# Performance work log

Measured on AMD Instinct MI355X. Metric: run time of the kernel, lower is better.

## Reference

```python
import jax, jax.numpy as jnp
import numpy as np


def setup_inputs() -> dict:
    key = jax.random.key(0)
    k1, k2, k3 = jax.random.split(key, 3)
    B, C, E = 65536, 32, 512
    candidate_ids = jax.random.randint(k1, (B, C), 0, E, dtype=jnp.int64)
    candidate_scores = jax.random.uniform(k2, (B, C), dtype=jnp.float32)
    cooc = jax.random.uniform(k3, (E, E), dtype=jnp.float32)
    # row-normalize like update_cooccurrence would maintain
    cooc = cooc / jnp.clip(cooc.sum(axis=1, keepdims=True), 1e-8)
    return {
        "candidate_ids": candidate_ids,
        "candidate_scores": candidate_scores,
        "cooccurrence": cooc,
        "target_size": 64,
    }


def reference(candidate_ids, candidate_scores, cooccurrence, target_size):
    B, C = candidate_ids.shape
    E = cooccurrence.shape[0]
    num_to_add = target_size - C  # static; original returns early if <= 0
    rows = jnp.arange(B)[:, None]  # [B,1]
    # sum_i score[b,i] * cooccurrence[ids[b,i]]  ==  scatter scores into [B,E], then matmul
    sparse_scores = jnp.zeros((B, E), jnp.float32).at[rows, candidate_ids].add(candidate_scores)
    cooc_scores = sparse_scores @ cooccurrence  # [B,E]
    # mask out existing candidates
    cooc_scores = cooc_scores.at[rows, candidate_ids].set(-jnp.inf)
    additional_scores, additional_ids = jax.lax.top_k(cooc_scores, num_to_add)
    expanded_ids = jnp.concatenate([candidate_ids, additional_ids.astype(candidate_ids.dtype)], axis=-1)
    expanded_scores = jnp.concatenate([candidate_scores, additional_scores], axis=-1)
    return expanded_ids, expanded_scores
```

## Files before the change

kernel.cpp:

```cpp
#include <hip/hip_runtime.h>
#include <stdint.h>

typedef unsigned long long u64;
typedef unsigned int u32;

constexpr int Ccand = 32;
constexpr int Evoc  = 512;
constexpr int Tgt   = 64;

__device__ __forceinline__ void sort64_desc_f32(float& a, int lane) {
    #pragma unroll
    for (int k2 = 2; k2 <= 64; k2 <<= 1) {
        #pragma unroll
        for (int j = k2 >> 1; j > 0; j >>= 1) {
            float o = __shfl_xor(a, j);
            bool lower = (lane & j) == 0;
            bool keepMax = ((lane & k2) == 0) ? lower : !lower;
            bool g = a > o;
            a = (keepMax == g) ? a : o;
        }
    }
}

__device__ __forceinline__ void sort64_desc_u64(u64& a, int lane) {
    #pragma unroll
    for (int k2 = 2; k2 <= 64; k2 <<= 1) {
        #pragma unroll
        for (int j = k2 >> 1; j > 0; j >>= 1) {
            u64 o = __shfl_xor(a, j);
            bool lower = (lane & j) == 0;
            bool keepMax = ((lane & k2) == 0) ? lower : !lower;
            bool g = a > o;
            a = (keepMax == g) ? a : o;
        }
    }
}

__global__ __launch_bounds__(256, 4) void cooc_expand(
    const int* __restrict__ cand_ids,
    const float* __restrict__ cand_scores,
    const float* __restrict__ cooc,
    float* __restrict__ out_ids,
    float* __restrict__ out_scores,
    int B)
{
    const int lane = threadIdx.x & 63;
    const int wid  = threadIdx.x >> 6;
    const int row  = blockIdx.x * 4 + wid;
    __shared__ u64 buf[4][512];
    __shared__ u32 wmask[4][16];
    if (row >= B) return;

    if (lane < 16) wmask[wid][lane] = 0u;

    int   my_id = -1;
    float my_s  = 0.0f;
    if (lane < Ccand) {
        my_id = cand_ids[(size_t)row * Ccand + lane];
        my_s  = cand_scores[(size_t)row * Ccand + lane];
    }

    int   first = 64;
    float sm    = 0.0f;
    #pragma unroll
    for (int j = 0; j < Ccand; ++j) {
        int   idj = __shfl(my_id, j);
        float sj  = __shfl(my_s,  j);
        bool match = (idj == my_id);
        if (match && j < first) first = j;
        sm += match ? sj : 0.0f;
    }
    bool alive = (lane < Ccand) && (first == lane);
    u64 aball = __ballot(alive);
    int m = __popcll(aball);

    __threadfence_block();
    if (alive) atomicOr(&wmask[wid][my_id >> 5], 1u << (my_id & 31));
    __threadfence_block();

    u32 wword = wmask[wid][lane & 15];
    u32 pc = __popc(wword);
    u32 incl = pc;
    #pragma unroll
    for (int i = 1; i < 16; i <<= 1) {
        u32 t2 = __shfl_up(incl, i);
        if (lane >= i) incl += t2;
    }
    u32 scanex = incl - pc;
    int W = (my_id >> 5) & 15;
    u32 basew = __shfl(scanex, W);
    u32 wordw = __shfl(wword, W);
    int rk = (int)basew + __popc(wordw & ((1u << (my_id & 31)) - 1u));

    int dst = alive ? rk : ((lane < 32) ? (lane + 32) : lane);
    int sorted_id = __builtin_amdgcn_ds_permute(dst << 2, my_id);
    int sorted_sb = __builtin_amdgcn_ds_permute(dst << 2, __float_as_int(sm));

    float acc[8] = {0.f,0.f,0.f,0.f,0.f,0.f,0.f,0.f};
    const int l4 = lane << 2;
    #pragma unroll 1
    for (int t = 0; t < 32; t += 8) {
        int   e[8];
        float s[8];
        #pragma unroll
        for (int u = 0; u < 8; ++u) {
            e[u] = __builtin_amdgcn_readlane(sorted_id, t + u) & 511;
            s[u] = (t + u < m) ? __int_as_float(__builtin_amdgcn_readlane(sorted_sb, t + u)) : 0.0f;
        }
        float4 A[8], Bv[8];
        #pragma unroll
        for (int u = 0; u < 8; ++u) {
            const float* rp = cooc + ((size_t)e[u] << 9);
            A[u]  = *reinterpret_cast<const float4*>(rp + l4);
            Bv[u] = *reinterpret_cast<const float4*>(rp + 256 + l4);
        }
        #pragma unroll
        for (int u = 0; u < 8; ++u) {
            acc[0] = fmaf(s[u], A[u].x,  acc[0]);
            acc[1] = fmaf(s[u], A[u].y,  acc[1]);
            acc[2] = fmaf(s[u], A[u].z,  acc[2]);
            acc[3] = fmaf(s[u], A[u].w,  acc[3]);
            acc[4] = fmaf(s[u], Bv[u].x, acc[4]);
            acc[5] = fmaf(s[u], Bv[u].y, acc[5]);
            acc[6] = fmaf(s[u], Bv[u].z, acc[6]);
            acc[7] = fmaf(s[u], Bv[u].w, acc[7]);
        }
    }

    u32 wlo = __shfl(wword, lane >> 3);
    u32 whi = __shfl(wword, 8 + (lane >> 3));
    int sh = (lane & 7) << 2;
    u32 flo = (wlo >> sh) & 0xFu;
    u32 fhi = (whi >> sh) & 0xFu;

    float v[8];
    #pragma unroll
    for (int j = 0; j < 4; ++j) {
        v[j]     = ((flo >> j) & 1u) ? -1.0f : acc[j];
        v[4 + j] = ((fhi >> j) & 1u) ? -1.0f : acc[4 + j];
    }

    float mx8 = v[0];
    #pragma unroll
    for (int j = 1; j < 8; ++j) mx8 = fmaxf(mx8, v[j]);
    float srt = mx8;
    sort64_desc_f32(srt, lane);
    float L32 = __int_as_float(__builtin_amdgcn_readlane(__float_as_int(srt), 31));

    int cnt = 0;
    #pragma unroll
    for (int j = 0; j < 8; ++j) cnt += (v[j] >= L32) ? 1 : 0;
    u32 sincl = (u32)cnt;
    #pragma unroll
    for (int i = 1; i < 64; i <<= 1) {
        u32 t2 = __shfl_up(sincl, i);
        if (lane >= i) sincl += t2;
    }
    int sbase = (int)sincl - cnt;
    int S_tot = __builtin_amdgcn_readlane((int)sincl, 63);

    int slot = sbase;
    #pragma unroll
    for (int j = 0; j < 8; ++j) {
        bool s = (v[j] >= L32);
        if (s) {
            int col = (j < 4) ? (l4 + j) : (256 + l4 + (j - 4));
            buf[wid][slot] = ((u64)__float_as_uint(v[j]) << 32) | (u32)(511 - col);
        }
        slot += s ? 1 : 0;
    }
    __threadfence_block();

    u64 k;
    if (S_tot <= 64) {
        k = (lane < S_tot) ? buf[wid][lane] : 0ull;
        sort64_desc_u64(k, lane);
    } else {
        u64 cur = (lane < S_tot) ? buf[wid][lane] : 0ull;
        sort64_desc_u64(cur, lane);
        for (int base = 64; base < S_tot; base += 64) {
            u64 nxt = (base + lane < S_tot) ? buf[wid][base + lane] : 0ull;
            sort64_desc_u64(nxt, lane);
            u64 o = __shfl_xor(nxt, 63);
            cur = (cur >= o) ? cur : o;
            #pragma unroll
            for (int j = 32; j > 0; j >>= 1) {
                u64 p = __shfl_xor(cur, j);
                bool keepMax = (lane & j) == 0;
                bool g = cur > p;
                cur = (keepMax == g) ? cur : p;
            }
        }
        k = cur;
    }

    int src = (lane >= 32) ? (lane - 32) : 0;
    u64 kk = __shfl(k, src);
    const size_t ob = (size_t)row * Tgt;
    float oid, osc;
    if (lane < Ccand) {
        oid = (float)my_id;
        osc = my_s;
    } else {
        oid = (float)(int)(511 - (u32)(kk & 511ull));
        osc = __uint_as_float((u32)(kk >> 32));
    }
    out_ids[ob + lane]    = oid;
    out_scores[ob + lane] = osc;
}

extern "C" void kernel_launch(void* const* d_in, const int* in_sizes, int n_in,
                              void* d_out, int out_size, void* d_ws, size_t ws_size,
                              hipStream_t stream) {
    const int*   ids    = (const int*)d_in[0];
    const float* scores = (const float*)d_in[1];
    const float* cooc   = (const float*)d_in[2];
    int B = in_sizes[0] / Ccand;
    float* out_ids    = (float*)d_out;
    float* out_scores = out_ids + (size_t)B * Tgt;
    int blocks = (B + 3) / 4;
    hipLaunchKernelGGL(cooc_expand, dim3(blocks), dim3(256), 0, stream,
                       ids, scores, cooc, out_ids, out_scores, B);
}
```

Baseline: 215.1 us.

## Replace LDS bitmask dedup with sort-based dedup and packed FMA accumulation

Candidate deduplication now uses a 32-lane bitonic sort on (id,lane) keys with neighbor checks, falling back to an O(C) shuffle path only when an id appears three or more times. This removes the shared-memory bitmask, its atomics and the fences. The accumulation uses float2 vector FMAs so the compiler can emit packed FMA instructions. The existing-candidate mask is now built per lane inside the gather loop. The trade-off is more shuffle work in the sort and a data-dependent branch.

```diff
diff --git a/kernel.cpp b/kernel.cpp
--- a/kernel.cpp
+++ b/kernel.cpp
@@ -3,6 +3,7 @@
 
 typedef unsigned long long u64;
 typedef unsigned int u32;
+typedef float vf2 __attribute__((ext_vector_type(2)));
 
 constexpr int Ccand = 32;
 constexpr int Evoc  = 512;
@@ -48,10 +49,7 @@
     const int wid  = threadIdx.x >> 6;
     const int row  = blockIdx.x * 4 + wid;
     __shared__ u64 buf[4][512];
-    __shared__ u32 wmask[4][16];
     if (row >= B) return;
-
-    if (lane < 16) wmask[wid][lane] = 0u;
 
     int   my_id = -1;
     float my_s  = 0.0f;
@@ -60,43 +58,80 @@
         my_s  = cand_scores[(size_t)row * Ccand + lane];
     }
 
-    int   first = 64;
-    float sm    = 0.0f;
-    #pragma unroll
-    for (int j = 0; j < Ccand; ++j) {
-        int   idj = __shfl(my_id, j);
-        float sj  = __shfl(my_s,  j);
-        bool match = (idj == my_id);
-        if (match && j < first) first = j;
-        sm += match ? sj : 0.0f;
-    }
-    bool alive = (lane < Ccand) && (first == lane);
-    u64 aball = __ballot(alive);
-    int m = __popcll(aball);
-
-    __threadfence_block();
-    if (alive) atomicOr(&wmask[wid][my_id >> 5], 1u << (my_id & 31));
-    __threadfence_block();
-
-    u32 wword = wmask[wid][lane & 15];
-    u32 pc = __popc(wword);
-    u32 incl = pc;
-    #pragma unroll
-    for (int i = 1; i < 16; i <<= 1) {
-        u32 t2 = __shfl_up(incl, i);
-        if (lane >= i) incl += t2;
-    }
-    u32 scanex = incl - pc;
-    int W = (my_id >> 5) & 15;
-    u32 basew = __shfl(scanex, W);
-    u32 wordw = __shfl(wword, W);
-    int rk = (int)basew + __popc(wordw & ((1u << (my_id & 31)) - 1u));
-
-    int dst = alive ? rk : ((lane < 32) ? (lane + 32) : lane);
-    int sorted_id = __builtin_amdgcn_ds_permute(dst << 2, my_id);
-    int sorted_sb = __builtin_amdgcn_ds_permute(dst << 2, __float_as_int(sm));
-
-    float acc[8] = {0.f,0.f,0.f,0.f,0.f,0.f,0.f,0.f};
+    u32   key = (lane < Ccand) ? (((u32)my_id << 5) | (u32)lane) : 0x7FFFFFFFu;
+    float sv  = my_s;
+    const int l5 = lane & 31;
+    #pragma unroll
+    for (int k2 = 2; k2 <= 32; k2 <<= 1) {
+        #pragma unroll
+        for (int j = k2 >> 1; j > 0; j >>= 1) {
+            u32   ok = __shfl_xor(key, j);
+            float os = __shfl_xor(sv, j);
+            bool lower   = (l5 & j) == 0;
+            bool keepMin = ((l5 & k2) == 0) ? lower : !lower;
+            bool g = key < ok;
+            bool keep = (g == keepMin);
+            key = keep ? key : ok;
+            sv  = keep ? sv  : os;
+        }
+    }
+    int sid = (int)(key >> 5);
+    u32 kprev  = __shfl_up(key, 1);
+    u32 kprev2 = __shfl_up(key, 2);
+    u32 knext  = __shfl_down(key, 1);
+    float snext = __shfl_down(sv, 1);
+    int idprev  = (int)(kprev  >> 5);
+    int idprev2 = (int)(kprev2 >> 5);
+    int idnext  = (int)(knext  >> 5);
+    bool isFirst = (lane == 0) || (sid != idprev);
+    bool hasPair = (lane < 31) && (idnext == sid);
+    float ssum = sv + (hasPair ? snext : 0.0f);
+    bool third = (lane >= 2) && (lane < Ccand) && (sid == idprev) && (sid == idprev2);
+    bool anyTriple = (__ballot(third) != 0ull);
+
+    int sorted_id, sorted_sb, m;
+    if (!anyTriple) {
+        bool flag = (lane < Ccand) && isFirst;
+        int f = flag ? 1 : 0;
+        u32 inc = (u32)f;
+        #pragma unroll
+        for (int i = 1; i < 64; i <<= 1) {
+            u32 t2 = __shfl_up(inc, i);
+            if (lane >= i) inc += t2;
+        }
+        m = __builtin_amdgcn_readlane((int)inc, 63);
+        int dstl = flag ? ((int)inc - 1) : 63;
+        sorted_id = __builtin_amdgcn_ds_permute(dstl << 2, sid);
+        sorted_sb = __builtin_amdgcn_ds_permute(dstl << 2, __float_as_int(ssum));
+    } else {
+        int first = 64; float sm = 0.0f;
+        #pragma unroll
+        for (int j = 0; j < Ccand; ++j) {
+            int   idj = __shfl(my_id, j);
+            float sj  = __shfl(my_s,  j);
+            bool match = (idj == my_id);
+            if (match && j < first) first = j;
+            sm += match ? sj : 0.0f;
+        }
+        bool alive = (lane < Ccand) && (first == lane);
+        u64 ab = __ballot(alive);
+        m = __popcll(ab);
+        int rk = 0;
+        #pragma unroll
+        for (int j = 0; j < Ccand; ++j) {
+            int idj = __shfl(my_id, j);
+            bool aj = (ab >> j) & 1ull;
+            rk += (aj && idj < my_id) ? 1 : 0;
+        }
+        int dstl = alive ? rk : ((lane < 32) ? (lane + 32) : lane);
+        sorted_id = __builtin_amdgcn_ds_permute(dstl << 2, my_id);
+        sorted_sb = __builtin_amdgcn_ds_permute(dstl << 2, __float_as_int(sm));
+    }
+
+    vf2 acc2[4];
+    acc2[0] = (vf2){0.f, 0.f}; acc2[1] = (vf2){0.f, 0.f};
+    acc2[2] = (vf2){0.f, 0.f}; acc2[3] = (vf2){0.f, 0.f};
+    u32 maskbits = 0;
     const int l4 = lane << 2;
     #pragma unroll 1
     for (int t = 0; t < 32; t += 8) {
@@ -116,29 +151,29 @@
         }
         #pragma unroll
         for (int u = 0; u < 8; ++u) {
-            acc[0] = fmaf(s[u], A[u].x,  acc[0]);
-            acc[1] = fmaf(s[u], A[u].y,  acc[1]);
-            acc[2] = fmaf(s[u], A[u].z,  acc[2]);
-            acc[3] = fmaf(s[u], A[u].w,  acc[3]);
-            acc[4] = fmaf(s[u], Bv[u].x, acc[4]);
-            acc[5] = fmaf(s[u], Bv[u].y, acc[5]);
-            acc[6] = fmaf(s[u], Bv[u].z, acc[6]);
-            acc[7] = fmaf(s[u], Bv[u].w, acc[7]);
-        }
-    }
-
-    u32 wlo = __shfl(wword, lane >> 3);
-    u32 whi = __shfl(wword, 8 + (lane >> 3));
-    int sh = (lane & 7) << 2;
-    u32 flo = (wlo >> sh) & 0xFu;
-    u32 fhi = (whi >> sh) & 0xFu;
+            vf2 sv2; sv2[0] = s[u]; sv2[1] = s[u];
+            vf2 a0; a0[0] = A[u].x;  a0[1] = A[u].y;
+            vf2 a1; a1[0] = A[u].z;  a1[1] = A[u].w;
+            vf2 b0; b0[0] = Bv[u].x; b0[1] = Bv[u].y;
+            vf2 b1; b1[0] = Bv[u].z; b1[1] = Bv[u].w;
+            acc2[0] = __builtin_elementwise_fma(sv2, a0, acc2[0]);
+            acc2[1] = __builtin_elementwise_fma(sv2, a1, acc2[1]);
+            acc2[2] = __builtin_elementwise_fma(sv2, b0, acc2[2]);
+            acc2[3] = __builtin_elementwise_fma(sv2, b1, acc2[3]);
+        }
+        #pragma unroll
+        for (int u = 0; u < 8; ++u) {
+            if ((t + u < m) && (((e[u] & 255) >> 2) == lane))
+                maskbits |= 1u << (((e[u] >> 8) << 2) | (e[u] & 3));
+        }
+    }
 
     float v[8];
-    #pragma unroll
-    for (int j = 0; j < 4; ++j) {
-        v[j]     = ((flo >> j) & 1u) ? -1.0f : acc[j];
-        v[4 + j] = ((fhi >> j) & 1u) ? -1.0f : acc[4 + j];
-    }
+    v[0] = acc2[0][0]; v[1] = acc2[0][1]; v[2] = acc2[1][0]; v[3] = acc2[1][1];
+    v[4] = acc2[2][0]; v[5] = acc2[2][1]; v[6] = acc2[3][0]; v[7] = acc2[3][1];
+    #pragma unroll
+    for (int j = 0; j < 8; ++j)
+        if ((maskbits >> j) & 1u) v[j] = -1.0f;
 
     float mx8 = v[0];
     #pragma unroll
```

New measurement: 226.4 us. +5.3%, slower.

## Shrink LDS footprint, compute ranks and exclusion mask in registers, use packed FMA

Applied to the files above, without the earlier changes.

Replaces the shared-memory bitmask and atomicOr ranking with a register-only rank computed by shuffles over the alive candidates. The exclusion mask is now built per lane inside the gather loop. The top-k staging buffer is cut from 512 to 64 entries per wave by processing the threshold survivors in 64-element chunks, and launch bounds move from 4 to 8 blocks per CU. The inner loop now loads 4 rows per step instead of 8 and uses packed 2-wide FMAs. The intent is higher occupancy through less LDS and register pressure, at the cost of fewer loads in flight per wave, a 32-step shuffle loop, and re-scanning candidates for each chunk when more than 64 survive.

```diff
diff --git a/kernel.cpp b/kernel.cpp
--- a/kernel.cpp
+++ b/kernel.cpp
@@ -3,6 +3,7 @@
 
 typedef unsigned long long u64;
 typedef unsigned int u32;
+typedef float vf2 __attribute__((ext_vector_type(2)));
 
 constexpr int Ccand = 32;
 constexpr int Evoc  = 512;
@@ -36,7 +37,7 @@
     }
 }
 
-__global__ __launch_bounds__(256, 4) void cooc_expand(
+__global__ __launch_bounds__(256, 8) void cooc_expand(
     const int* __restrict__ cand_ids,
     const float* __restrict__ cand_scores,
     const float* __restrict__ cooc,
@@ -47,11 +48,8 @@
     const int lane = threadIdx.x & 63;
     const int wid  = threadIdx.x >> 6;
     const int row  = blockIdx.x * 4 + wid;
-    __shared__ u64 buf[4][512];
-    __shared__ u32 wmask[4][16];
+    __shared__ u64 buf[4][64];
     if (row >= B) return;
-
-    if (lane < 16) wmask[wid][lane] = 0u;
 
     int   my_id = -1;
     float my_s  = 0.0f;
@@ -74,71 +72,63 @@
     u64 aball = __ballot(alive);
     int m = __popcll(aball);
 
-    __threadfence_block();
-    if (alive) atomicOr(&wmask[wid][my_id >> 5], 1u << (my_id & 31));
-    __threadfence_block();
-
-    u32 wword = wmask[wid][lane & 15];
-    u32 pc = __popc(wword);
-    u32 incl = pc;
-    #pragma unroll
-    for (int i = 1; i < 16; i <<= 1) {
-        u32 t2 = __shfl_up(incl, i);
-        if (lane >= i) incl += t2;
-    }
-    u32 scanex = incl - pc;
-    int W = (my_id >> 5) & 15;
-    u32 basew = __shfl(scanex, W);
-    u32 wordw = __shfl(wword, W);
-    int rk = (int)basew + __popc(wordw & ((1u << (my_id & 31)) - 1u));
-
+    int rk = 0;
+    #pragma unroll
+    for (int j = 0; j < Ccand; ++j) {
+        int idj = __shfl(my_id, j);
+        bool aj = (aball >> j) & 1ull;
+        rk += (aj && idj < my_id) ? 1 : 0;
+    }
     int dst = alive ? rk : ((lane < 32) ? (lane + 32) : lane);
     int sorted_id = __builtin_amdgcn_ds_permute(dst << 2, my_id);
     int sorted_sb = __builtin_amdgcn_ds_permute(dst << 2, __float_as_int(sm));
 
-    float acc[8] = {0.f,0.f,0.f,0.f,0.f,0.f,0.f,0.f};
+    vf2 acc2[4];
+    acc2[0] = (vf2){0.f, 0.f}; acc2[1] = (vf2){0.f, 0.f};
+    acc2[2] = (vf2){0.f, 0.f}; acc2[3] = (vf2){0.f, 0.f};
+    u32 maskbits = 0;
     const int l4 = lane << 2;
     #pragma unroll 1
-    for (int t = 0; t < 32; t += 8) {
-        int   e[8];
-        float s[8];
-        #pragma unroll
-        for (int u = 0; u < 8; ++u) {
+    for (int t = 0; t < 32; t += 4) {
+        int   e[4];
+        float s[4];
+        #pragma unroll
+        for (int u = 0; u < 4; ++u) {
             e[u] = __builtin_amdgcn_readlane(sorted_id, t + u) & 511;
             s[u] = (t + u < m) ? __int_as_float(__builtin_amdgcn_readlane(sorted_sb, t + u)) : 0.0f;
         }
-        float4 A[8], Bv[8];
-        #pragma unroll
-        for (int u = 0; u < 8; ++u) {
+        float4 A[4], Bv[4];
+        #pragma unroll
+        for (int u = 0; u < 4; ++u) {
             const float* rp = cooc + ((size_t)e[u] << 9);
             A[u]  = *reinterpret_cast<const float4*>(rp + l4);
             Bv[u] = *reinterpret_cast<const float4*>(rp + 256 + l4);
         }
         #pragma unroll
-        for (int u = 0; u < 8; ++u) {
-            acc[0] = fmaf(s[u], A[u].x,  acc[0]);
-            acc[1] = fmaf(s[u], A[u].y,  acc[1]);
-            acc[2] = fmaf(s[u], A[u].z,  acc[2]);
-            acc[3] = fmaf(s[u], A[u].w,  acc[3]);
-            acc[4] = fmaf(s[u], Bv[u].x, acc[4]);
-            acc[5] = fmaf(s[u], Bv[u].y, acc[5]);
-            acc[6] = fmaf(s[u], Bv[u].z, acc[6]);
-            acc[7] = fmaf(s[u], Bv[u].w, acc[7]);
-        }
-    }
-
-    u32 wlo = __shfl(wword, lane >> 3);
-    u32 whi = __shfl(wword, 8 + (lane >> 3));
-    int sh = (lane & 7) << 2;
-    u32 flo = (wlo >> sh) & 0xFu;
-    u32 fhi = (whi >> sh) & 0xFu;
+        for (int u = 0; u < 4; ++u) {
+            vf2 sv2; sv2[0] = s[u]; sv2[1] = s[u];
+            vf2 a0; a0[0] = A[u].x;  a0[1] = A[u].y;
+            vf2 a1; a1[0] = A[u].z;  a1[1] = A[u].w;
+            vf2 b0; b0[0] = Bv[u].x; b0[1] = Bv[u].y;
+            vf2 b1; b1[0] = Bv[u].z; b1[1] = Bv[u].w;
+            acc2[0] = __builtin_elementwise_fma(sv2, a0, acc2[0]);
+            acc2[1] = __builtin_elementwise_fma(sv2, a1, acc2[1]);
+            acc2[2] = __builtin_elementwise_fma(sv2, b0, acc2[2]);
+            acc2[3] = __builtin_elementwise_fma(sv2, b1, acc2[3]);
+        }
+        #pragma unroll
+        for (int u = 0; u < 4; ++u) {
+            if ((t + u < m) && (((e[u] & 255) >> 2) == lane))
+                maskbits |= 1u << (((e[u] >> 8) << 2) | (e[u] & 3));
+        }
+    }
 
     float v[8];
-    #pragma unroll
-    for (int j = 0; j < 4; ++j) {
-        v[j]     = ((flo >> j) & 1u) ? -1.0f : acc[j];
-        v[4 + j] = ((fhi >> j) & 1u) ? -1.0f : acc[4 + j];
-    }
+    v[0] = acc2[0][0]; v[1] = acc2[0][1]; v[2] = acc2[1][0]; v[3] = acc2[1][1];
+    v[4] = acc2[2][0]; v[5] = acc2[2][1]; v[6] = acc2[3][0]; v[7] = acc2[3][1];
+    #pragma unroll
+    for (int j = 0; j < 8; ++j)
+        if ((maskbits >> j) & 1u) v[j] = -1.0f;
 
     float mx8 = v[0];
     #pragma unroll
@@ -159,28 +149,29 @@
     int sbase = (int)sincl - cnt;
     int S_tot = __builtin_amdgcn_readlane((int)sincl, 63);
 
-    int slot = sbase;
-    #pragma unroll
-    for (int j = 0; j < 8; ++j) {
-        bool s = (v[j] >= L32);
-        if (s) {
-            int col = (j < 4) ? (l4 + j) : (256 + l4 + (j - 4));
-            buf[wid][slot] = ((u64)__float_as_uint(v[j]) << 32) | (u32)(511 - col);
-        }
-        slot += s ? 1 : 0;
-    }
-    __threadfence_block();
-
-    u64 k;
-    if (S_tot <= 64) {
-        k = (lane < S_tot) ? buf[wid][lane] : 0ull;
-        sort64_desc_u64(k, lane);
-    } else {
-        u64 cur = (lane < S_tot) ? buf[wid][lane] : 0ull;
-        sort64_desc_u64(cur, lane);
-        for (int base = 64; base < S_tot; base += 64) {
-            u64 nxt = (base + lane < S_tot) ? buf[wid][base + lane] : 0ull;
-            sort64_desc_u64(nxt, lane);
+    int nchunk = (S_tot + 63) >> 6;
+    u64 cur = 0ull;
+    #pragma unroll 1
+    for (int c = 0; c < nchunk; ++c) {
+        const int lo = c << 6;
+        int slot = sbase;
+        #pragma unroll
+        for (int j = 0; j < 8; ++j) {
+            bool s = (v[j] >= L32);
+            int  rel = slot - lo;
+            if (s && rel >= 0 && rel < 64) {
+                int col = (j < 4) ? (l4 + j) : (256 + l4 + (j - 4));
+                buf[wid][rel] = ((u64)__float_as_uint(v[j]) << 32) | (u32)(511 - col);
+            }
+            slot += s ? 1 : 0;
+        }
+        __threadfence_block();
+        u64 nxt = (lo + lane < S_tot) ? buf[wid][lane] : 0ull;
+        __threadfence_block();
+        sort64_desc_u64(nxt, lane);
+        if (c == 0) {
+            cur = nxt;
+        } else {
             u64 o = __shfl_xor(nxt, 63);
             cur = (cur >= o) ? cur : o;
             #pragma unroll
@@ -191,11 +182,10 @@
                 cur = (keepMax == g) ? cur : p;
             }
         }
-        k = cur;
     }
 
     int src = (lane >= 32) ? (lane - 32) : 0;
-    u64 kk = __shfl(k, src);
+    u64 kk = __shfl(cur, src);
     const size_t ob = (size_t)row * Tgt;
     float oid, osc;
     if (lane < Ccand) {
```

New measurement: 209.7 us. 2.5% less time.
